# Performance work log

Measured on AMD Instinct MI355X. Metric: run time of the kernel, lower is better.

Reference implementation:

```python
import jax, jax.numpy as jnp
import numpy as np

N_NODES = 100000
N_EDGES = 1600000
D = 64
K = 10


def setup_inputs() -> dict:
    key = jax.random.key(0)
    k1, k2, k3, k4 = jax.random.split(key, 4)
    features = jax.random.normal(k1, (N_NODES, D), dtype=jnp.float32)
    s = jax.random.normal(k2, (D, 1), dtype=jnp.float32)
    src = jax.random.randint(k3, (N_EDGES,), 0, N_NODES, dtype=jnp.int64)
    dst = jax.random.randint(k4, (N_EDGES,), 0, N_NODES, dtype=jnp.int64)
    return {"features": features, "s": s, "src": src, "dst": dst, "k": K}


def reference(features, s, src, dst, k):
    n = features.shape[0]
    # symmetric degree norm: deg_in clamped at 1, norm = deg^{-1/2}
    deg = jax.ops.segment_sum(jnp.ones_like(dst, dtype=features.dtype), dst,
                              num_segments=n)
    norm = jnp.power(jnp.maximum(deg, 1.0), -0.5)[:, None]  # [N,1]

    def step(h, _):
        h = h * norm
        # copy_u + sum: scatter-add src features into dst nodes (SpMM)
        h = jax.ops.segment_sum(h[src], dst, num_segments=n)
        h = h * norm
        return h, h

    _, hops = jax.lax.scan(step, features, None, length=k)  # [k,N,D]
    H = jnp.concatenate([features[None], hops], axis=0)      # [k+1,N,D]
    H = jnp.transpose(H, (1, 0, 2))                           # [N,k+1,D]
    # attention pooling: S = sigmoid(H @ s), out = S^T H
    S = jax.nn.sigmoid(jnp.einsum('nkd,d->nk', H, s[:, 0]))  # [N,k+1]
    out = jnp.einsum('nk,nkd->nd', S, H)                      # [N,D]
    return out
```

## Files before the change

### kernel.cpp

```cpp
#include <hip/hip_runtime.h>
#include <hip/hip_fp16.h>
#include <math.h>

#define D 64
#define RB 1024
#define EB 2048
#define NRMAX 128
#define KHOPS 10


typedef union { uint4 u; __half2 h[4]; } U4H;


__global__ void countA(const int* __restrict__ dst, int* __restrict__ countsA_T,
                       int E, int NR, int NBLK) {
    __shared__ int hist[NRMAX];
    int t = threadIdx.x;
    for (int i = t; i < NR; i += 256) hist[i] = 0;
    __syncthreads();
    int base = blockIdx.x * EB + t;
    #pragma unroll
    for (int j = 0; j < EB / 256; ++j) {
        int e = base + j * 256;
        if (e < E) atomicAdd(&hist[dst[e] >> 10], 1);
    }
    __syncthreads();
    for (int i = t; i < NR; i += 256) countsA_T[i * NBLK + blockIdx.x] = hist[i];
}

__global__ void block_sums(const int* __restrict__ arr, int* __restrict__ bsum, int n) {
    int base = blockIdx.x * 1024;
    int t = threadIdx.x;
    int v = 0;
    #pragma unroll
    for (int j = 0; j < 4; ++j) {
        int i = base + t + j * 256;
        if (i < n) v += arr[i];
    }
    #pragma unroll
    for (int m = 32; m >= 1; m >>= 1) v += __shfl_xor(v, m, 64);
    __shared__ int ws[4];
    if ((t & 63) == 0) ws[t >> 6] = v;
    __syncthreads();
    if (t == 0) bsum[blockIdx.x] = ws[0] + ws[1] + ws[2] + ws[3];
}

__global__ void scan_bsums(int* __restrict__ bsum, int nb) {
    __shared__ int tmp[1024];
    int t = threadIdx.x;
    int v = (t < nb) ? bsum[t] : 0;
    tmp[t] = v;
    __syncthreads();
    for (int off = 1; off < 1024; off <<= 1) {
        int x = (t >= off) ? tmp[t - off] : 0;
        __syncthreads();
        tmp[t] += x;
        __syncthreads();
    }
    if (t < nb) bsum[t] = tmp[t] - v;
}

__global__ void gen_scan2(const int* __restrict__ arr, const int* __restrict__ bsum,
                          int* __restrict__ out, int n) {
    __shared__ int tmp[1024];
    int base = blockIdx.x * 1024;
    int t = threadIdx.x;
    int i = base + t;
    int v = (i < n) ? arr[i] : 0;
    tmp[t] = v;
    __syncthreads();
    for (int off = 1; off < 1024; off <<= 1) {
        int x = (t >= off) ? tmp[t - off] : 0;
        __syncthreads();
        tmp[t] += x;
        __syncthreads();
    }
    if (i < n) out[i] = bsum[blockIdx.x] + tmp[t] - v;
}

__global__ void passA2(const int* __restrict__ src, const int* __restrict__ dst,
                       const int* __restrict__ baseA, unsigned int* __restrict__ ebuf2,
                       int E, int NR, int NBLK) {
    __shared__ int cur[NRMAX];
    int t = threadIdx.x;
    for (int i = t; i < NR; i += 256) cur[i] = baseA[i * NBLK + blockIdx.x];
    __syncthreads();
    int base = blockIdx.x * EB + t;
    #pragma unroll
    for (int j = 0; j < EB / 256; ++j) {
        int e = base + j * 256;
        if (e < E) {
            int v = dst[e];
            int pos = atomicAdd(&cur[v >> 10], 1);
            ebuf2[pos] = (unsigned int)src[e] | ((unsigned int)(v & (RB - 1)) << 17);
        }
    }
}

__global__ void range_build(const unsigned int* __restrict__ ebuf2,
                            const int* __restrict__ baseA,
                            int* __restrict__ offsets, float* __restrict__ norm,
                            int* __restrict__ csr, int N, int E, int NR, int NBLK) {
    __shared__ int cnt[RB];
    __shared__ int sc[RB];
    int rg = blockIdx.x;
    int t = threadIdx.x;
    int r0 = baseA[rg * NBLK];
    int r1 = (rg + 1 < NR) ? baseA[(rg + 1) * NBLK] : E;
    cnt[t] = 0;
    __syncthreads();
    for (int i = r0 + t; i < r1; i += RB)
        atomicAdd(&cnt[ebuf2[i] >> 17], 1);
    __syncthreads();
    int v = cnt[t];
    sc[t] = v;
    __syncthreads();
    for (int off = 1; off < RB; off <<= 1) {
        int x = (t >= off) ? sc[t - off] : 0;
        __syncthreads();
        sc[t] += x;
        __syncthreads();
    }
    int excl = sc[t] - v;
    int node = rg * RB + t;
    if (node < N) {
        offsets[node] = r0 + excl;
        norm[node] = rsqrtf((float)(v > 1 ? v : 1));
    }
    if (rg == NR - 1 && t == 0) offsets[N] = E;
    __syncthreads();
    cnt[t] = r0 + excl;
    __syncthreads();
    for (int i = r0 + t; i < r1; i += RB) {
        unsigned int u = ebuf2[i];
        int pos = atomicAdd(&cnt[u >> 17], 1);
        csr[pos] = (int)(u & 0x1FFFFu);
    }
}


__global__ void hop0(const float4* __restrict__ feat, const float* __restrict__ s,
                     const float* __restrict__ norm, uint4* __restrict__ g0,
                     float4* __restrict__ out, int n, int do_pool) {
    int t = blockIdx.x * blockDim.x + threadIdx.x;
    int node = t >> 3;
    int l = t & 7;
    if (node > n) return;
    if (node == n) {
        g0[(size_t)n * 8 + l] = make_uint4(0u, 0u, 0u, 0u);
        return;
    }
    float4 f0 = feat[node * 16 + 2 * l];
    float4 f1 = feat[node * 16 + 2 * l + 1];
    float nv = norm[node];
    U4H P;
    P.h[0] = __floats2half2_rn(f0.x * nv, f0.y * nv);
    P.h[1] = __floats2half2_rn(f0.z * nv, f0.w * nv);
    P.h[2] = __floats2half2_rn(f1.x * nv, f1.y * nv);
    P.h[3] = __floats2half2_rn(f1.z * nv, f1.w * nv);
    g0[(size_t)node * 8 + l] = P.u;
    if (do_pool) {
        const float4* s4 = (const float4*)s;
        float4 a = s4[2 * l], b = s4[2 * l + 1];
        float dot = f0.x * a.x + f0.y * a.y + f0.z * a.z + f0.w * a.w
                  + f1.x * b.x + f1.y * b.y + f1.z * b.z + f1.w * b.w;
        #pragma unroll
        for (int m = 1; m <= 4; m <<= 1) dot += __shfl_xor(dot, m, 64);
        float sig = 1.0f / (1.0f + expf(-dot));
        out[node * 16 + 2 * l]     = make_float4(sig * f0.x, sig * f0.y, sig * f0.z, sig * f0.w);
        out[node * 16 + 2 * l + 1] = make_float4(sig * f1.x, sig * f1.y, sig * f1.z, sig * f1.w);
    }
}


__global__ void spmm_hop(const uint4* __restrict__ gin, const int* __restrict__ offsets,
                         const int* __restrict__ csr, const float* __restrict__ norm,
                         const float* __restrict__ s, uint4* __restrict__ gout,
                         float4* __restrict__ out, int n, int do_pool, int write_g) {
    int lane = threadIdx.x & 63;
    int node = __builtin_amdgcn_readfirstlane(blockIdx.x * 4 + (threadIdx.x >> 6));
    if (node > n) return;
    int g = lane >> 3;
    int l = lane & 7;
    if (node == n) {
        if (write_g && g == 0) gout[(size_t)n * 8 + l] = make_uint4(0u, 0u, 0u, 0u);
        return;
    }
    int beg = offsets[node], end = offsets[node + 1];
    int deg = end - beg;
    int dcap = deg < 64 ? deg : 64;
    int idx = (lane < dcap) ? csr[beg + lane] : n;
    int nr = (dcap + 7) >> 3;

    __half2 z = __floats2half2_rn(0.f, 0.f);
    __half2 ah0 = z, ah1 = z, ah2 = z, ah3 = z;
    U4H A0, A1, A2, A3, A4, A5, A6, A7;
    if (nr > 0) { int u = __shfl(idx, g,      64); A0.u = gin[(size_t)u * 8 + l]; }
    if (nr > 1) { int u = __shfl(idx, g + 8,  64); A1.u = gin[(size_t)u * 8 + l]; }
    if (nr > 2) { int u = __shfl(idx, g + 16, 64); A2.u = gin[(size_t)u * 8 + l]; }
    if (nr > 3) { int u = __shfl(idx, g + 24, 64); A3.u = gin[(size_t)u * 8 + l]; }
    if (nr > 4) { int u = __shfl(idx, g + 32, 64); A4.u = gin[(size_t)u * 8 + l]; }
    if (nr > 5) { int u = __shfl(idx, g + 40, 64); A5.u = gin[(size_t)u * 8 + l]; }
    if (nr > 6) { int u = __shfl(idx, g + 48, 64); A6.u = gin[(size_t)u * 8 + l]; }
    if (nr > 7) { int u = __shfl(idx, g + 56, 64); A7.u = gin[(size_t)u * 8 + l]; }
    if (nr > 0) { ah0 = __hadd2(ah0, A0.h[0]); ah1 = __hadd2(ah1, A0.h[1]); ah2 = __hadd2(ah2, A0.h[2]); ah3 = __hadd2(ah3, A0.h[3]); }
    if (nr > 1) { ah0 = __hadd2(ah0, A1.h[0]); ah1 = __hadd2(ah1, A1.h[1]); ah2 = __hadd2(ah2, A1.h[2]); ah3 = __hadd2(ah3, A1.h[3]); }
    if (nr > 2) { ah0 = __hadd2(ah0, A2.h[0]); ah1 = __hadd2(ah1, A2.h[1]); ah2 = __hadd2(ah2, A2.h[2]); ah3 = __hadd2(ah3, A2.h[3]); }
    if (nr > 3) { ah0 = __hadd2(ah0, A3.h[0]); ah1 = __hadd2(ah1, A3.h[1]); ah2 = __hadd2(ah2, A3.h[2]); ah3 = __hadd2(ah3, A3.h[3]); }
    if (nr > 4) { ah0 = __hadd2(ah0, A4.h[0]); ah1 = __hadd2(ah1, A4.h[1]); ah2 = __hadd2(ah2, A4.h[2]); ah3 = __hadd2(ah3, A4.h[3]); }
    if (nr > 5) { ah0 = __hadd2(ah0, A5.h[0]); ah1 = __hadd2(ah1, A5.h[1]); ah2 = __hadd2(ah2, A5.h[2]); ah3 = __hadd2(ah3, A5.h[3]); }
    if (nr > 6) { ah0 = __hadd2(ah0, A6.h[0]); ah1 = __hadd2(ah1, A6.h[1]); ah2 = __hadd2(ah2, A6.h[2]); ah3 = __hadd2(ah3, A6.h[3]); }
    if (nr > 7) { ah0 = __hadd2(ah0, A7.h[0]); ah1 = __hadd2(ah1, A7.h[1]); ah2 = __hadd2(ah2, A7.h[2]); ah3 = __hadd2(ah3, A7.h[3]); }

    float2 q0 = __half22float2(ah0), q1 = __half22float2(ah1);
    float2 q2 = __half22float2(ah2), q3 = __half22float2(ah3);
    float acc[8] = {q0.x, q0.y, q1.x, q1.y, q2.x, q2.y, q3.x, q3.y};

    for (int i = beg + 64 + g; i < end; i += 8) {
        U4H P; P.u = gin[(size_t)csr[i] * 8 + l];
        float2 a0 = __half22float2(P.h[0]), a1 = __half22float2(P.h[1]);
        float2 a2 = __half22float2(P.h[2]), a3 = __half22float2(P.h[3]);
        acc[0] += a0.x; acc[1] += a0.y; acc[2] += a1.x; acc[3] += a1.y;
        acc[4] += a2.x; acc[5] += a2.y; acc[6] += a3.x; acc[7] += a3.y;
    }

    #pragma unroll
    for (int m = 8; m <= 32; m <<= 1) {
        #pragma unroll
        for (int jj = 0; jj < 8; ++jj) acc[jj] += __shfl_xor(acc[jj], m, 64);
    }

    float nv = norm[node];
    float h[8];
    #pragma unroll
    for (int jj = 0; jj < 8; ++jj) h[jj] = acc[jj] * nv;

    float sig = 0.f;
    if (do_pool) {
        const float4* s4 = (const float4*)s;
        float4 a = s4[2 * l], b = s4[2 * l + 1];
        float dot = h[0] * a.x + h[1] * a.y + h[2] * a.z + h[3] * a.w
                  + h[4] * b.x + h[5] * b.y + h[6] * b.z + h[7] * b.w;
        #pragma unroll
        for (int m = 1; m <= 4; m <<= 1) dot += __shfl_xor(dot, m, 64);
        sig = 1.0f / (1.0f + expf(-dot));
    }

    if (g == 0) {
        if (write_g) {
            U4H P;
            P.h[0] = __floats2half2_rn(h[0] * nv, h[1] * nv);
            P.h[1] = __floats2half2_rn(h[2] * nv, h[3] * nv);
            P.h[2] = __floats2half2_rn(h[4] * nv, h[5] * nv);
            P.h[3] = __floats2half2_rn(h[6] * nv, h[7] * nv);
            gout[(size_t)node * 8 + l] = P.u;
        }
        if (do_pool) {
            float4 o0 = out[node * 16 + 2 * l];
            float4 o1 = out[node * 16 + 2 * l + 1];
            o0.x += sig * h[0]; o0.y += sig * h[1]; o0.z += sig * h[2]; o0.w += sig * h[3];
            o1.x += sig * h[4]; o1.y += sig * h[5]; o1.z += sig * h[6]; o1.w += sig * h[7];
            out[node * 16 + 2 * l]     = o0;
            out[node * 16 + 2 * l + 1] = o1;
        }
    }
}


__global__ void pool_epilogue(const uint4* __restrict__ gbase, size_t gstride,
                              const float* __restrict__ norm,
                              const float* __restrict__ s,
                              float4* __restrict__ out, int N) {
    int t0 = blockIdx.x * blockDim.x + threadIdx.x;
    int node = t0 >> 3;
    int l = t0 & 7;
    if (node >= N) return;
    float inv_nv = 1.0f / norm[node];
    const float4* s4 = (const float4*)s;
    float4 sa = s4[2 * l], sb = s4[2 * l + 1];
    float o[8] = {0.f, 0.f, 0.f, 0.f, 0.f, 0.f, 0.f, 0.f};
    for (int t = 0; t <= KHOPS; ++t) {
        U4H P; P.u = gbase[(size_t)t * gstride + (size_t)node * 8 + l];
        float2 a0 = __half22float2(P.h[0]), a1 = __half22float2(P.h[1]);
        float2 a2 = __half22float2(P.h[2]), a3 = __half22float2(P.h[3]);
        float gf[8] = {a0.x, a0.y, a1.x, a1.y, a2.x, a2.y, a3.x, a3.y};
        float dot = gf[0] * sa.x + gf[1] * sa.y + gf[2] * sa.z + gf[3] * sa.w
                  + gf[4] * sb.x + gf[5] * sb.y + gf[6] * sb.z + gf[7] * sb.w;
        #pragma unroll
        for (int m = 1; m <= 4; m <<= 1) dot += __shfl_xor(dot, m, 64);
        float sig = 1.0f / (1.0f + expf(-dot * inv_nv));
        float sc = sig * inv_nv;
        #pragma unroll
        for (int j = 0; j < 8; ++j) o[j] += sc * gf[j];
    }
    out[node * 16 + 2 * l]     = make_float4(o[0], o[1], o[2], o[3]);
    out[node * 16 + 2 * l + 1] = make_float4(o[4], o[5], o[6], o[7]);
}


extern "C" void kernel_launch(void* const* d_in, const int* in_sizes, int n_in,
                              void* d_out, int out_size, void* d_ws, size_t ws_size,
                              hipStream_t stream) {
    const float* feat = (const float*)d_in[0];
    const float* s    = (const float*)d_in[1];
    const int*   src  = (const int*)d_in[2];
    const int*   dst  = (const int*)d_in[3];

    int N = in_sizes[0] / D;
    int E = in_sizes[2];
    int NR   = (N + RB - 1) / RB;
    int NBLK = (E + EB - 1) / EB;
    int M    = NR * NBLK;
    int nchA = (M + 1023) / 1024;

    int*   offsets  = (int*)d_ws;
    int*   csr      = offsets + (N + 1);
    float* norm     = (float*)(csr + E);
    int*   countsA  = (int*)(norm + N);
    int*   baseA    = countsA + M;
    int*   bsumA    = baseA + M;
    uintptr_t p = (uintptr_t)(bsumA + nchA);
    p = (p + 255) & ~(uintptr_t)255;
    uint4* gbase = (uint4*)p;
    size_t gstride = (size_t)(N + 1) * 8;

    size_t fixed_bytes = (uintptr_t)gbase - (uintptr_t)d_ws;
    int deferred = (ws_size >= fixed_bytes + (size_t)(KHOPS + 1) * gstride * sizeof(uint4)) ? 1 : 0;

    unsigned int* ebuf2 = (unsigned int*)(gbase + gstride);

    countA<<<NBLK, 256, 0, stream>>>(dst, countsA, E, NR, NBLK);
    block_sums<<<nchA, 256, 0, stream>>>(countsA, bsumA, M);
    scan_bsums<<<1, 1024, 0, stream>>>(bsumA, nchA);
    gen_scan2<<<nchA, 1024, 0, stream>>>(countsA, bsumA, baseA, M);
    passA2<<<NBLK, 256, 0, stream>>>(src, dst, baseA, ebuf2, E, NR, NBLK);
    range_build<<<NR, RB, 0, stream>>>(ebuf2, baseA, offsets, norm, csr, N, E, NR, NBLK);

    float4* outp = (float4*)d_out;
    int nb_node8 = ((N + 1) * 8 + 255) / 256;
    int nb_spmm  = (N + 4) / 4;

    hop0<<<nb_node8, 256, 0, stream>>>((const float4*)feat, s, norm, gbase,
                                       outp, N, deferred ? 0 : 1);

    if (deferred) {
        for (int t = 0; t < KHOPS; ++t) {
            spmm_hop<<<nb_spmm, 256, 0, stream>>>(
                gbase + (size_t)t * gstride, offsets, csr, norm, s,
                gbase + (size_t)(t + 1) * gstride, outp, N, 0, 1);
        }
        pool_epilogue<<<nb_node8, 256, 0, stream>>>(gbase, gstride, norm, s, outp, N);
    } else {
        uint4* gin = gbase;
        uint4* gout = gbase + gstride;
        for (int t = 0; t < KHOPS; ++t) {
            spmm_hop<<<nb_spmm, 256, 0, stream>>>(
                gin, offsets, csr, norm, s, gout, outp, N, 1, (t < KHOPS - 1) ? 1 : 0);
            uint4* tmp = gin; gin = gout; gout = tmp;
        }
    }
}
```

Baseline: 547.4 us.

## Process four nodes per wavefront in SpMM hop to raise memory parallelism

Each wavefront now handles four destination nodes instead of one. It loads up to 32 neighbour indices per node, using half-wave index loads, and issues all the gathers for the four nodes before any accumulation. The goal is fewer idle lanes (average degree is about 16, so most of a 64-lane index load was wasted) and more outstanding loads per wave. In exchange, register pressure rises from the 16 buffered uint4 loads and four accumulator sets, launch_bounds is set to 256 threads with 4 blocks, and grid size drops by four.

```diff
diff --git a/kernel.cpp b/kernel.cpp
--- a/kernel.cpp
+++ b/kernel.cpp
@@ -173,97 +173,134 @@
 }
 
 
-__global__ void spmm_hop(const uint4* __restrict__ gin, const int* __restrict__ offsets,
-                         const int* __restrict__ csr, const float* __restrict__ norm,
-                         const float* __restrict__ s, uint4* __restrict__ gout,
-                         float4* __restrict__ out, int n, int do_pool, int write_g) {
+#define ACCUM_NODE(K, BUF, ACC)                                               \
+    {                                                                         \
+        __half2 h0 = z, h1 = z, h2 = z, h3 = z;                               \
+        if (nr[K] > 0) { h0 = __hadd2(h0, BUF[0].h[0]); h1 = __hadd2(h1, BUF[0].h[1]); h2 = __hadd2(h2, BUF[0].h[2]); h3 = __hadd2(h3, BUF[0].h[3]); } \
+        if (nr[K] > 1) { h0 = __hadd2(h0, BUF[1].h[0]); h1 = __hadd2(h1, BUF[1].h[1]); h2 = __hadd2(h2, BUF[1].h[2]); h3 = __hadd2(h3, BUF[1].h[3]); } \
+        if (nr[K] > 2) { h0 = __hadd2(h0, BUF[2].h[0]); h1 = __hadd2(h1, BUF[2].h[1]); h2 = __hadd2(h2, BUF[2].h[2]); h3 = __hadd2(h3, BUF[2].h[3]); } \
+        if (nr[K] > 3) { h0 = __hadd2(h0, BUF[3].h[0]); h1 = __hadd2(h1, BUF[3].h[1]); h2 = __hadd2(h2, BUF[3].h[2]); h3 = __hadd2(h3, BUF[3].h[3]); } \
+        float2 q0 = __half22float2(h0), q1 = __half22float2(h1);              \
+        float2 q2 = __half22float2(h2), q3 = __half22float2(h3);              \
+        ACC[0] = q0.x; ACC[1] = q0.y; ACC[2] = q1.x; ACC[3] = q1.y;           \
+        ACC[4] = q2.x; ACC[5] = q2.y; ACC[6] = q3.x; ACC[7] = q3.y;           \
+        for (int i = beg[K] + 32 + g; i < beg[K] + deg[K]; i += 8) {          \
+            U4H P; P.u = gin[(size_t)csr[i] * 8 + l];                         \
+            float2 b0 = __half22float2(P.h[0]), b1 = __half22float2(P.h[1]);  \
+            float2 b2 = __half22float2(P.h[2]), b3 = __half22float2(P.h[3]);  \
+            ACC[0] += b0.x; ACC[1] += b0.y; ACC[2] += b1.x; ACC[3] += b1.y;   \
+            ACC[4] += b2.x; ACC[5] += b2.y; ACC[6] += b3.x; ACC[7] += b3.y;   \
+        }                                                                     \
+    }
+
+#define STORE_NODE(K, ACC)                                                    \
+    {                                                                         \
+        int nd = nb + K;                                                      \
+        if (nd < n) {                                                         \
+            float nv = norm[nd];                                              \
+            float h0 = ACC[0] * nv, h1 = ACC[1] * nv, h2 = ACC[2] * nv, h3 = ACC[3] * nv; \
+            float h4 = ACC[4] * nv, h5 = ACC[5] * nv, h6 = ACC[6] * nv, h7 = ACC[7] * nv; \
+            float sig = 0.f;                                                  \
+            if (do_pool) {                                                    \
+                float dot = h0 * sa.x + h1 * sa.y + h2 * sa.z + h3 * sa.w     \
+                          + h4 * sb.x + h5 * sb.y + h6 * sb.z + h7 * sb.w;    \
+                _Pragma("unroll")                                             \
+                for (int m = 1; m <= 4; m <<= 1) dot += __shfl_xor(dot, m, 64); \
+                sig = 1.0f / (1.0f + expf(-dot));                             \
+            }                                                                 \
+            if (g == 0) {                                                     \
+                if (write_g) {                                                \
+                    U4H P;                                                    \
+                    P.h[0] = __floats2half2_rn(h0 * nv, h1 * nv);             \
+                    P.h[1] = __floats2half2_rn(h2 * nv, h3 * nv);             \
+                    P.h[2] = __floats2half2_rn(h4 * nv, h5 * nv);             \
+                    P.h[3] = __floats2half2_rn(h6 * nv, h7 * nv);             \
+                    gout[(size_t)nd * 8 + l] = P.u;                           \
+                }                                                             \
+                if (do_pool) {                                                \
+                    float4 o0 = out[nd * 16 + 2 * l];                         \
+                    float4 o1 = out[nd * 16 + 2 * l + 1];                     \
+                    o0.x += sig * h0; o0.y += sig * h1; o0.z += sig * h2; o0.w += sig * h3; \
+                    o1.x += sig * h4; o1.y += sig * h5; o1.z += sig * h6; o1.w += sig * h7; \
+                    out[nd * 16 + 2 * l]     = o0;                            \
+                    out[nd * 16 + 2 * l + 1] = o1;                            \
+                }                                                             \
+            }                                                                 \
+        } else if (nd == n && write_g && g == 0) {                            \
+            gout[(size_t)n * 8 + l] = make_uint4(0u, 0u, 0u, 0u);             \
+        }                                                                     \
+    }
+
+__global__ __launch_bounds__(256, 4)
+void spmm_hop(const uint4* __restrict__ gin, const int* __restrict__ offsets,
+              const int* __restrict__ csr, const float* __restrict__ norm,
+              const float* __restrict__ s, uint4* __restrict__ gout,
+              float4* __restrict__ out, int n, int do_pool, int write_g) {
     int lane = threadIdx.x & 63;
-    int node = __builtin_amdgcn_readfirstlane(blockIdx.x * 4 + (threadIdx.x >> 6));
-    if (node > n) return;
+    int wv = threadIdx.x >> 6;
+    int nb = __builtin_amdgcn_readfirstlane((int)blockIdx.x * 16 + wv * 4);
+    if (nb > n) return;
     int g = lane >> 3;
     int l = lane & 7;
-    if (node == n) {
-        if (write_g && g == 0) gout[(size_t)n * 8 + l] = make_uint4(0u, 0u, 0u, 0u);
-        return;
-    }
-    int beg = offsets[node], end = offsets[node + 1];
-    int deg = end - beg;
-    int dcap = deg < 64 ? deg : 64;
-    int idx = (lane < dcap) ? csr[beg + lane] : n;
-    int nr = (dcap + 7) >> 3;
+
+    int beg[4], deg[4], nr[4];
+    #pragma unroll
+    for (int k = 0; k < 4; ++k) {
+        int nd = nb + k;
+        int b = 0, e = 0;
+        if (nd < n) { b = offsets[nd]; e = offsets[nd + 1]; }
+        beg[k] = b;
+        deg[k] = e - b;
+        int dc = deg[k] < 32 ? deg[k] : 32;
+        nr[k] = (dc + 7) >> 3;
+    }
+
+    int e31 = lane & 31;
+    int hi = lane >> 5;
+    int bA = hi ? beg[1] : beg[0];
+    int cA = hi ? (deg[1] < 32 ? deg[1] : 32) : (deg[0] < 32 ? deg[0] : 32);
+    int idxA = (e31 < cA) ? csr[bA + e31] : n;
+    int bB = hi ? beg[3] : beg[2];
+    int cB = hi ? (deg[3] < 32 ? deg[3] : 32) : (deg[2] < 32 ? deg[2] : 32);
+    int idxB = (e31 < cB) ? csr[bB + e31] : n;
+
+    U4H B0[4], B1[4], B2[4], B3[4];
+    #pragma unroll
+    for (int r = 0; r < 4; ++r) {
+        if (nr[0] > r) { int u = __shfl(idxA, r * 8 + g, 64);      B0[r].u = gin[(size_t)u * 8 + l]; }
+        if (nr[1] > r) { int u = __shfl(idxA, 32 + r * 8 + g, 64); B1[r].u = gin[(size_t)u * 8 + l]; }
+        if (nr[2] > r) { int u = __shfl(idxB, r * 8 + g, 64);      B2[r].u = gin[(size_t)u * 8 + l]; }
+        if (nr[3] > r) { int u = __shfl(idxB, 32 + r * 8 + g, 64); B3[r].u = gin[(size_t)u * 8 + l]; }
+    }
 
     __half2 z = __floats2half2_rn(0.f, 0.f);
-    __half2 ah0 = z, ah1 = z, ah2 = z, ah3 = z;
-    U4H A0, A1, A2, A3, A4, A5, A6, A7;
-    if (nr > 0) { int u = __shfl(idx, g,      64); A0.u = gin[(size_t)u * 8 + l]; }
-    if (nr > 1) { int u = __shfl(idx, g + 8,  64); A1.u = gin[(size_t)u * 8 + l]; }
-    if (nr > 2) { int u = __shfl(idx, g + 16, 64); A2.u = gin[(size_t)u * 8 + l]; }
-    if (nr > 3) { int u = __shfl(idx, g + 24, 64); A3.u = gin[(size_t)u * 8 + l]; }
-    if (nr > 4) { int u = __shfl(idx, g + 32, 64); A4.u = gin[(size_t)u * 8 + l]; }
-    if (nr > 5) { int u = __shfl(idx, g + 40, 64); A5.u = gin[(size_t)u * 8 + l]; }
-    if (nr > 6) { int u = __shfl(idx, g + 48, 64); A6.u = gin[(size_t)u * 8 + l]; }
-    if (nr > 7) { int u = __shfl(idx, g + 56, 64); A7.u = gin[(size_t)u * 8 + l]; }
-    if (nr > 0) { ah0 = __hadd2(ah0, A0.h[0]); ah1 = __hadd2(ah1, A0.h[1]); ah2 = __hadd2(ah2, A0.h[2]); ah3 = __hadd2(ah3, A0.h[3]); }
-    if (nr > 1) { ah0 = __hadd2(ah0, A1.h[0]); ah1 = __hadd2(ah1, A1.h[1]); ah2 = __hadd2(ah2, A1.h[2]); ah3 = __hadd2(ah3, A1.h[3]); }
-    if (nr > 2) { ah0 = __hadd2(ah0, A2.h[0]); ah1 = __hadd2(ah1, A2.h[1]); ah2 = __hadd2(ah2, A2.h[2]); ah3 = __hadd2(ah3, A2.h[3]); }
-    if (nr > 3) { ah0 = __hadd2(ah0, A3.h[0]); ah1 = __hadd2(ah1, A3.h[1]); ah2 = __hadd2(ah2, A3.h[2]); ah3 = __hadd2(ah3, A3.h[3]); }
-    if (nr > 4) { ah0 = __hadd2(ah0, A4.h[0]); ah1 = __hadd2(ah1, A4.h[1]); ah2 = __hadd2(ah2, A4.h[2]); ah3 = __hadd2(ah3, A4.h[3]); }
-    if (nr > 5) { ah0 = __hadd2(ah0, A5.h[0]); ah1 = __hadd2(ah1, A5.h[1]); ah2 = __hadd2(ah2, A5.h[2]); ah3 = __hadd2(ah3, A5.h[3]); }
-    if (nr > 6) { ah0 = __hadd2(ah0, A6.h[0]); ah1 = __hadd2(ah1, A6.h[1]); ah2 = __hadd2(ah2, A6.h[2]); ah3 = __hadd2(ah3, A6.h[3]); }
-    if (nr > 7) { ah0 = __hadd2(ah0, A7.h[0]); ah1 = __hadd2(ah1, A7.h[1]); ah2 = __hadd2(ah2, A7.h[2]); ah3 = __hadd2(ah3, A7.h[3]); }
-
-    float2 q0 = __half22float2(ah0), q1 = __half22float2(ah1);
-    float2 q2 = __half22float2(ah2), q3 = __half22float2(ah3);
-    float acc[8] = {q0.x, q0.y, q1.x, q1.y, q2.x, q2.y, q3.x, q3.y};
-
-    for (int i = beg + 64 + g; i < end; i += 8) {
-        U4H P; P.u = gin[(size_t)csr[i] * 8 + l];
-        float2 a0 = __half22float2(P.h[0]), a1 = __half22float2(P.h[1]);
-        float2 a2 = __half22float2(P.h[2]), a3 = __half22float2(P.h[3]);
-        acc[0] += a0.x; acc[1] += a0.y; acc[2] += a1.x; acc[3] += a1.y;
-        acc[4] += a2.x; acc[5] += a2.y; acc[6] += a3.x; acc[7] += a3.y;
-    }
+    float acc0[8], acc1[8], acc2[8], acc3[8];
+    ACCUM_NODE(0, B0, acc0)
+    ACCUM_NODE(1, B1, acc1)
+    ACCUM_NODE(2, B2, acc2)
+    ACCUM_NODE(3, B3, acc3)
 
     #pragma unroll
     for (int m = 8; m <= 32; m <<= 1) {
         #pragma unroll
-        for (int jj = 0; jj < 8; ++jj) acc[jj] += __shfl_xor(acc[jj], m, 64);
-    }
-
-    float nv = norm[node];
-    float h[8];
-    #pragma unroll
-    for (int jj = 0; jj < 8; ++jj) h[jj] = acc[jj] * nv;
-
-    float sig = 0.f;
+        for (int jj = 0; jj < 8; ++jj) {
+            acc0[jj] += __shfl_xor(acc0[jj], m, 64);
+            acc1[jj] += __shfl_xor(acc1[jj], m, 64);
+            acc2[jj] += __shfl_xor(acc2[jj], m, 64);
+            acc3[jj] += __shfl_xor(acc3[jj], m, 64);
+        }
+    }
+
+    float4 sa = make_float4(0.f, 0.f, 0.f, 0.f), sb = sa;
     if (do_pool) {
         const float4* s4 = (const float4*)s;
-        float4 a = s4[2 * l], b = s4[2 * l + 1];
-        float dot = h[0] * a.x + h[1] * a.y + h[2] * a.z + h[3] * a.w
-                  + h[4] * b.x + h[5] * b.y + h[6] * b.z + h[7] * b.w;
-        #pragma unroll
-        for (int m = 1; m <= 4; m <<= 1) dot += __shfl_xor(dot, m, 64);
-        sig = 1.0f / (1.0f + expf(-dot));
-    }
-
-    if (g == 0) {
-        if (write_g) {
-            U4H P;
-            P.h[0] = __floats2half2_rn(h[0] * nv, h[1] * nv);
-            P.h[1] = __floats2half2_rn(h[2] * nv, h[3] * nv);
-            P.h[2] = __floats2half2_rn(h[4] * nv, h[5] * nv);
-            P.h[3] = __floats2half2_rn(h[6] * nv, h[7] * nv);
-            gout[(size_t)node * 8 + l] = P.u;
-        }
-        if (do_pool) {
-            float4 o0 = out[node * 16 + 2 * l];
-            float4 o1 = out[node * 16 + 2 * l + 1];
-            o0.x += sig * h[0]; o0.y += sig * h[1]; o0.z += sig * h[2]; o0.w += sig * h[3];
-            o1.x += sig * h[4]; o1.y += sig * h[5]; o1.z += sig * h[6]; o1.w += sig * h[7];
-            out[node * 16 + 2 * l]     = o0;
-            out[node * 16 + 2 * l + 1] = o1;
-        }
-    }
+        sa = s4[2 * l]; sb = s4[2 * l + 1];
+    }
+
+    STORE_NODE(0, acc0)
+    STORE_NODE(1, acc1)
+    STORE_NODE(2, acc2)
+    STORE_NODE(3, acc3)
 }
 
 
@@ -338,7 +375,7 @@
 
     float4* outp = (float4*)d_out;
     int nb_node8 = ((N + 1) * 8 + 255) / 256;
-    int nb_spmm  = (N + 4) / 4;
+    int nb_spmm  = (N + 16) / 16;
 
     hop0<<<nb_node8, 256, 0, stream>>>((const float4*)feat, s, norm, gbase,
                                        outp, N, deferred ? 0 : 1);
```

After: 629.8 us. +15.0%, slower.
